# Kernel tuning notes

Hardware: AMD Instinct MI355X
Metric: run time of the kernel (lower is better)

## Reference

```python
import jax, jax.numpy as jnp
import numpy as np

N_NODES = 8_000_000
N_GRAPHS = 16384
OUT_DIM = 256
LABEL_MAX = 300  # some labels >= OUT_DIM to exercise the bounds check


def setup_inputs() -> dict:
    key = jax.random.key(0)
    k1, k2 = jax.random.split(key)
    x = jax.random.randint(k1, (N_NODES,), 0, LABEL_MAX, dtype=jnp.int32)
    # ptr: sorted segment boundaries with ptr[0]=0, ptr[-1]=N_NODES
    inner = jnp.sort(jax.random.randint(k2, (N_GRAPHS - 1,), 0, N_NODES, dtype=jnp.int32))
    ptr = jnp.concatenate([jnp.zeros((1,), jnp.int32), inner,
                           jnp.full((1,), N_NODES, jnp.int32)])
    node_weights = jnp.ones((N_NODES,), jnp.float32)  # all-ones -> plain counting
    return {"x": x, "ptr": ptr, "node_weights": node_weights,
            "num_graphs": N_GRAPHS, "out_dim": OUT_DIM}


def reference(x, ptr, node_weights, num_graphs, out_dim):
    # Segmented histogram: out[g, c] = # nodes in graph g with label c (c < out_dim).
    n = x.shape[0]
    # graph id of each node from CSR ptr boundaries
    seg = jnp.searchsorted(ptr, jnp.arange(n, dtype=ptr.dtype), side="right") - 1
    valid = x < out_dim
    xc = jnp.where(valid, x, 0)                 # clamp out-of-range labels
    w = jnp.where(valid, node_weights, 0.0)     # mask them out of the count
    out = jnp.zeros((num_graphs, out_dim), jnp.float32).at[seg, xc].add(w)
    return out
```

## Files before the change

### kernel.cpp

```cpp
#include <hip/hip_runtime.h>


extern "C" __global__ void seg_hist_kernel(const int* __restrict__ x,
                                           const int* __restrict__ ptr,
                                           const float* __restrict__ w,
                                           float* __restrict__ out,
                                           int out_dim) {
    extern __shared__ float hist[];

    const int g = blockIdx.x;
    const int start = ptr[g];
    const int end = ptr[g + 1];

    for (int c = threadIdx.x; c < out_dim; c += blockDim.x) hist[c] = 0.0f;
    __syncthreads();

    for (int i = start + (int)threadIdx.x; i < end; i += (int)blockDim.x) {
        const int lbl = x[i];
        if ((unsigned)lbl < (unsigned)out_dim) {
            atomicAdd(&hist[lbl], w[i]);
        }
    }
    __syncthreads();

    float* o = out + (size_t)g * (size_t)out_dim;
    for (int c = threadIdx.x; c < out_dim; c += blockDim.x) o[c] = hist[c];
}

extern "C" void kernel_launch(void* const* d_in, const int* in_sizes, int n_in,
                              void* d_out, int out_size, void* d_ws, size_t ws_size,
                              hipStream_t stream) {
    const int* x   = (const int*)d_in[0];
    const int* ptr = (const int*)d_in[1];
    const float* w = (const float*)d_in[2];
    float* out     = (float*)d_out;

    const int num_graphs = in_sizes[1] - 1;
    const int out_dim    = out_size / num_graphs;

    dim3 grid(num_graphs);
    dim3 block(256);
    size_t lds_bytes = (size_t)out_dim * sizeof(float);

    seg_hist_kernel<<<grid, block, lds_bytes, stream>>>(x, ptr, w, out, out_dim);
}
```

Baseline: 52.05 us.

## Partition histogram work by fixed node chunks with atomic merges at boundaries

Replaces the one-block-per-graph histogram with blocks that each own a fixed 2048-node chunk. A setup kernel binary-searches ptr for each chunk's starting graph and zeroes those rows. The main kernel stages x and w into LDS with vector loads, then walks the graphs overlapping its chunk. Graphs fully inside a chunk get their rows written directly; graphs cut by a chunk edge are merged with global atomics. This balances work regardless of segment sizes and widens loads, at the cost of an extra launch, per-graph barriers inside each chunk, and boundary atomics. A ws-size fallback keeps the old kernel.

```diff
diff --git a/kernel.cpp b/kernel.cpp
--- a/kernel.cpp
+++ b/kernel.cpp
@@ -1,30 +1,104 @@
 #include <hip/hip_runtime.h>
 
 
-extern "C" __global__ void seg_hist_kernel(const int* __restrict__ x,
-                                           const int* __restrict__ ptr,
-                                           const float* __restrict__ w,
-                                           float* __restrict__ out,
-                                           int out_dim) {
-    extern __shared__ float hist[];
+#define CHUNK   2048
+#define BLOCK_B 256
 
+extern "C" __global__ __launch_bounds__(64)
+void setup_kernel(const int* __restrict__ ptr, int* __restrict__ gstart,
+                  float* __restrict__ out, int n_nodes, int num_graphs,
+                  int out_dim) {
+    const int b = blockIdx.x;
+    long n0 = (long)b * CHUNK;
+    if (n0 > (long)n_nodes - 1) n0 = (long)n_nodes - 1;
+
+    int lo = 0, hi = num_graphs + 1;
+    while (lo < hi) {
+        const int mid = (lo + hi) >> 1;
+        if ((long)ptr[mid] <= n0) lo = mid + 1; else hi = mid;
+    }
+    const int g = lo - 1;
+
+    if (threadIdx.x == 0) gstart[b] = g;
+
+    float* row = out + (size_t)g * (size_t)out_dim;
+    for (int c = (int)threadIdx.x; c < out_dim; c += 64) row[c] = 0.0f;
+}
+
+extern "C" __global__ __launch_bounds__(BLOCK_B)
+void hist_kernel(const int* __restrict__ x, const int* __restrict__ ptr,
+                 const float* __restrict__ w, const int* __restrict__ gstart,
+                 float* __restrict__ out, int n_nodes, int out_dim) {
+    extern __shared__ char smem[];
+    int*   xbuf = (int*)smem;
+    float* wbuf = (float*)(smem + CHUNK * sizeof(int));
+    float* hist = (float*)(smem + CHUNK * sizeof(int) + CHUNK * sizeof(float));
+
+    const int b   = blockIdx.x;
+    const int t   = (int)threadIdx.x;
+    const int n0  = b * CHUNK;
+    const int n1  = min(n0 + CHUNK, n_nodes);
+    const int cnt = n1 - n0;
+
+    for (int base = 0; base < cnt; base += 4 * BLOCK_B) {
+        const int idx = base + t * 4;
+        if (idx + 4 <= cnt) {
+            *reinterpret_cast<int4*>(&xbuf[idx])   = *reinterpret_cast<const int4*>(&x[n0 + idx]);
+            *reinterpret_cast<float4*>(&wbuf[idx]) = *reinterpret_cast<const float4*>(&w[n0 + idx]);
+        } else if (idx < cnt) {
+            for (int k = idx; k < cnt; ++k) { xbuf[k] = x[n0 + k]; wbuf[k] = w[n0 + k]; }
+        }
+    }
+
+    const int g0 = gstart[b];
+    const int g1 = gstart[b + 1];
+    __syncthreads();
+
+    int pjs = ptr[g0];
+    for (int j = g0; j <= g1; ++j) {
+        const int pje = ptr[j + 1];
+        const int s = max(pjs, n0) - n0;
+        const int e = min(pje, n1) - n0;
+
+        for (int c = t; c < out_dim; c += BLOCK_B) hist[c] = 0.0f;
+        __syncthreads();
+
+        for (int i = s + t; i < e; i += BLOCK_B) {
+            const unsigned lbl = (unsigned)xbuf[i];
+            if (lbl < (unsigned)out_dim) atomicAdd(&hist[lbl], wbuf[i]);
+        }
+        __syncthreads();
+
+        float* row = out + (size_t)j * (size_t)out_dim;
+        if (j == g0 || j == g1) {
+            for (int c = t; c < out_dim; c += BLOCK_B) {
+                const float v = hist[c];
+                if (v != 0.0f) atomicAdd(&row[c], v);
+            }
+        } else {
+            for (int c = t; c < out_dim; c += BLOCK_B) row[c] = hist[c];
+        }
+        pjs = pje;
+    }
+}
+
+extern "C" __global__ __launch_bounds__(256)
+void seg_hist_fallback(const int* __restrict__ x, const int* __restrict__ ptr,
+                       const float* __restrict__ w, float* __restrict__ out,
+                       int out_dim) {
+    extern __shared__ float fhist[];
     const int g = blockIdx.x;
     const int start = ptr[g];
     const int end = ptr[g + 1];
-
-    for (int c = threadIdx.x; c < out_dim; c += blockDim.x) hist[c] = 0.0f;
+    for (int c = (int)threadIdx.x; c < out_dim; c += 256) fhist[c] = 0.0f;
     __syncthreads();
-
-    for (int i = start + (int)threadIdx.x; i < end; i += (int)blockDim.x) {
+    for (int i = start + (int)threadIdx.x; i < end; i += 256) {
         const int lbl = x[i];
-        if ((unsigned)lbl < (unsigned)out_dim) {
-            atomicAdd(&hist[lbl], w[i]);
-        }
+        if ((unsigned)lbl < (unsigned)out_dim) atomicAdd(&fhist[lbl], w[i]);
     }
     __syncthreads();
-
     float* o = out + (size_t)g * (size_t)out_dim;
-    for (int c = threadIdx.x; c < out_dim; c += blockDim.x) o[c] = hist[c];
+    for (int c = (int)threadIdx.x; c < out_dim; c += 256) o[c] = fhist[c];
 }
 
 extern "C" void kernel_launch(void* const* d_in, const int* in_sizes, int n_in,
@@ -35,12 +109,23 @@
     const float* w = (const float*)d_in[2];
     float* out     = (float*)d_out;
 
+    const int n_nodes    = in_sizes[0];
     const int num_graphs = in_sizes[1] - 1;
     const int out_dim    = out_size / num_graphs;
+    const int n_chunks   = (n_nodes + CHUNK - 1) / CHUNK;
 
-    dim3 grid(num_graphs);
-    dim3 block(256);
-    size_t lds_bytes = (size_t)out_dim * sizeof(float);
+    if (ws_size < (size_t)(n_chunks + 1) * sizeof(int)) {
+        seg_hist_fallback<<<num_graphs, 256, (size_t)out_dim * sizeof(float), stream>>>(
+            x, ptr, w, out, out_dim);
+        return;
+    }
 
-    seg_hist_kernel<<<grid, block, lds_bytes, stream>>>(x, ptr, w, out, out_dim);
+    int* gstart = (int*)d_ws;
+
+    setup_kernel<<<n_chunks + 1, 64, 0, stream>>>(ptr, gstart, out,
+                                                  n_nodes, num_graphs, out_dim);
+
+    const size_t lds = (size_t)CHUNK * 8 + (size_t)out_dim * sizeof(float);
+    hist_kernel<<<n_chunks, BLOCK_B, lds, stream>>>(x, ptr, w, gstart, out,
+                                                    n_nodes, out_dim);
 }
```

After: 57.45 us. +10.4%, slower.

## Partition nodes into fixed per-wave ranges with segment flush and double-buffered loads

Applied to the files above, without the earlier changes.

Replaces the one-block-per-graph kernel with a persistent grid where each wave takes a fixed 512-node range. The wave finds the owning graph by binary search over ptr using scalar loads, bins its nodes into a private LDS histogram, and writes each row directly when the graph lies wholly inside the range, otherwise merges it with global atomics. Vectorized int4/float4 loads are double-buffered across ranges, and the output is zeroed with a memset first. The aim is to remove the load imbalance from uneven segment sizes and to improve memory throughput, at the cost of an extra memset and boundary atomics.

```diff
diff --git a/kernel.cpp b/kernel.cpp
--- a/kernel.cpp
+++ b/kernel.cpp
@@ -1,30 +1,132 @@
 #include <hip/hip_runtime.h>
 
 
-extern "C" __global__ void seg_hist_kernel(const int* __restrict__ x,
-                                           const int* __restrict__ ptr,
-                                           const float* __restrict__ w,
-                                           float* __restrict__ out,
-                                           int out_dim) {
-    extern __shared__ float hist[];
+#define NPT   8
+#define WR    (64 * NPT)
+#define ODIM  256
+#define NBLK  1536
 
+__device__ __forceinline__ int sload_i32(const int* p, int idx) {
+    int v;
+    asm volatile("s_load_dword %0, %1, %2\n\ts_waitcnt lgkmcnt(0)"
+                 : "=&s"(v)
+                 : "s"(p), "s"(idx * 4));
+    return v;
+}
+
+#define LOADR(LA, LB, WA, WB, RR)                                              \
+    { const int _base = (RR) * WR + lane * NPT;                                \
+      if (_base + NPT <= n_nodes) {                                            \
+          LA = *reinterpret_cast<const int4*>(x + _base);                      \
+          LB = *reinterpret_cast<const int4*>(x + _base + 4);                  \
+          WA = *reinterpret_cast<const float4*>(w + _base);                    \
+          WB = *reinterpret_cast<const float4*>(w + _base + 4);                \
+      } else {                                                                 \
+          int _l[8]; float _w[8];                                              \
+          _Pragma("unroll")                                                    \
+          for (int _k = 0; _k < 8; ++_k) {                                     \
+              if (_base + _k < n_nodes) { _l[_k] = x[_base + _k];              \
+                                          _w[_k] = w[_base + _k]; }            \
+              else { _l[_k] = 0x7fffffff; _w[_k] = 0.0f; }                     \
+          }                                                                    \
+          LA = make_int4(_l[0], _l[1], _l[2], _l[3]);                          \
+          LB = make_int4(_l[4], _l[5], _l[6], _l[7]);                          \
+          WA = make_float4(_w[0], _w[1], _w[2], _w[3]);                        \
+          WB = make_float4(_w[4], _w[5], _w[6], _w[7]);                        \
+      } }
+
+#define ADDK(LBL, WV, K)                                                       \
+    { const int _n = nbase + (K);                                              \
+      if (_n >= s && _n < e && (unsigned)(LBL) < (unsigned)ODIM)               \
+          atomicAdd(&h[LBL], (WV)); }
+
+#define BINR(LA, LB, WA, WB, RR)                                               \
+    { const int r0 = __builtin_amdgcn_readfirstlane((RR) * WR);                \
+      const int r1 = min(r0 + WR, n_nodes);                                    \
+      const int nbase = r0 + lane * NPT;                                       \
+                  \
+      int lo = 0, hi = num_graphs - 1;                                         \
+      while (lo < hi) {                                                        \
+          const int mid = (lo + hi + 1) >> 1;                                  \
+          if (sload_i32(ptr, mid) <= r0) lo = mid; else hi = mid - 1;          \
+      }                                                                        \
+      int j = lo;                                                              \
+      int pstart = sload_i32(ptr, j);                                          \
+      for (;;) {                                                               \
+          const int pend = sload_i32(ptr, j + 1);                              \
+          const int s = max(pstart, r0);                                       \
+          const int e = min(pend, r1);                                         \
+          ADDK(LA.x, WA.x, 0) ADDK(LA.y, WA.y, 1)                              \
+          ADDK(LA.z, WA.z, 2) ADDK(LA.w, WA.w, 3)                              \
+          ADDK(LB.x, WB.x, 4) ADDK(LB.y, WB.y, 5)                              \
+          ADDK(LB.z, WB.z, 6) ADDK(LB.w, WB.w, 7)                              \
+          const bool whole = (pstart >= r0) && (pend <= r1);                   \
+          float* row = out + (size_t)j * ODIM;                                 \
+          _Pragma("unroll")                                                    \
+          for (int _k = 0; _k < 4; ++_k) {                                     \
+              const int bin = lane + 64 * _k;                                  \
+              const float v = h[bin];                                          \
+              if (whole)          row[bin] = v;                                \
+              else if (v != 0.0f) atomicAdd(&row[bin], v);                     \
+              h[bin] = 0.0f;                                                   \
+          }                                                                    \
+          if (pend >= r1) break;                                               \
+          ++j; pstart = pend;                                                  \
+      } }
+
+extern "C" __global__ __launch_bounds__(256, 6)
+void hist_kernel(const int* __restrict__ x, const int* __restrict__ ptr,
+                 const float* __restrict__ w, float* __restrict__ out,
+                 int n_nodes, int num_graphs) {
+    __shared__ float hist[4][ODIM];
+
+    const int wv   = (int)threadIdx.x >> 6;
+    const int lane = (int)threadIdx.x & 63;
+    float* h = hist[wv];
+
+#pragma unroll
+    for (int k = 0; k < 4; ++k) h[lane + 64 * k] = 0.0f;
+
+    const int n_ranges = (n_nodes + WR - 1) / WR;
+    const int stride   = NBLK * 4;
+    int r = (int)blockIdx.x * 4 + wv;
+
+    int4 la_a, lb_a, la_b, lb_b;
+    float4 wa_a, wb_a, wa_b, wb_b;
+
+    if (r < n_ranges) LOADR(la_a, lb_a, wa_a, wb_a, r);
+    bool useA = true;
+    while (r < n_ranges) {
+        const int rn = r + stride;
+        if (useA) {
+            if (rn < n_ranges) LOADR(la_b, lb_b, wa_b, wb_b, rn);
+            BINR(la_a, lb_a, wa_a, wb_a, r);
+        } else {
+            if (rn < n_ranges) LOADR(la_a, lb_a, wa_a, wb_a, rn);
+            BINR(la_b, lb_b, wa_b, wb_b, r);
+        }
+        useA = !useA;
+        r = rn;
+    }
+}
+
+extern "C" __global__ __launch_bounds__(256)
+void seg_hist_fallback(const int* __restrict__ x, const int* __restrict__ ptr,
+                       const float* __restrict__ w, float* __restrict__ out,
+                       int out_dim) {
+    extern __shared__ float fhist[];
     const int g = blockIdx.x;
     const int start = ptr[g];
     const int end = ptr[g + 1];
-
-    for (int c = threadIdx.x; c < out_dim; c += blockDim.x) hist[c] = 0.0f;
+    for (int c = (int)threadIdx.x; c < out_dim; c += 256) fhist[c] = 0.0f;
     __syncthreads();
-
-    for (int i = start + (int)threadIdx.x; i < end; i += (int)blockDim.x) {
+    for (int i = start + (int)threadIdx.x; i < end; i += 256) {
         const int lbl = x[i];
-        if ((unsigned)lbl < (unsigned)out_dim) {
-            atomicAdd(&hist[lbl], w[i]);
-        }
+        if ((unsigned)lbl < (unsigned)out_dim) atomicAdd(&fhist[lbl], w[i]);
     }
     __syncthreads();
-
     float* o = out + (size_t)g * (size_t)out_dim;
-    for (int c = threadIdx.x; c < out_dim; c += blockDim.x) o[c] = hist[c];
+    for (int c = (int)threadIdx.x; c < out_dim; c += 256) o[c] = fhist[c];
 }
 
 extern "C" void kernel_launch(void* const* d_in, const int* in_sizes, int n_in,
@@ -35,12 +137,17 @@
     const float* w = (const float*)d_in[2];
     float* out     = (float*)d_out;
 
+    const int n_nodes    = in_sizes[0];
     const int num_graphs = in_sizes[1] - 1;
     const int out_dim    = out_size / num_graphs;
 
-    dim3 grid(num_graphs);
-    dim3 block(256);
-    size_t lds_bytes = (size_t)out_dim * sizeof(float);
+    if (out_dim != ODIM) {
+        seg_hist_fallback<<<num_graphs, 256, (size_t)out_dim * sizeof(float), stream>>>(
+            x, ptr, w, out, out_dim);
+        return;
+    }
 
-    seg_hist_kernel<<<grid, block, lds_bytes, stream>>>(x, ptr, w, out, out_dim);
+    hipMemsetAsync(d_out, 0, (size_t)out_size * sizeof(float), stream);
+
+    hist_kernel<<<NBLK, 256, 0, stream>>>(x, ptr, w, out, n_nodes, num_graphs);
 }
```

Measured after the change: 59.60 us. +14.5%, slower.

## Split work into fixed node tiles per wavefront with per-wave LDS histograms

Applied to the files above, without the earlier changes.

Replaces one-block-per-graph scheduling with fixed 2048-node tiles, each handled by a single wavefront with its own LDS histogram. The wavefront finds the owning graph with a scalar binary search over ptr, then walks the segments inside its tile. A graph lying wholly inside a tile is written directly, while a boundary segment is merged into global memory with atomics after a memset of the output. The aim is to fix the load imbalance from uneven graph sizes and to use vectorized loads, at the cost of a memset launch, extra global atomics and per-segment flush overhead when tiles hold many small graphs.

```diff
diff --git a/kernel.cpp b/kernel.cpp
--- a/kernel.cpp
+++ b/kernel.cpp
@@ -1,30 +1,127 @@
 #include <hip/hip_runtime.h>
 
 
-extern "C" __global__ void seg_hist_kernel(const int* __restrict__ x,
-                                           const int* __restrict__ ptr,
-                                           const float* __restrict__ w,
-                                           float* __restrict__ out,
-                                           int out_dim) {
-    extern __shared__ float hist[];
+#define TILE  2048
+#define ODIM  256
 
+__device__ __forceinline__ int sload_i32(const int* p, int idx) {
+    const int off = __builtin_amdgcn_readfirstlane(idx * 4);
+    int v;
+    asm volatile("s_load_dword %0, %1, %2\n\ts_waitcnt lgkmcnt(0)"
+                 : "=&s"(v)
+                 : "s"(p), "s"(off));
+    return v;
+}
+
+extern "C" __global__ __launch_bounds__(256, 4)
+void hist_kernel(const int* __restrict__ x, const int* __restrict__ ptr,
+                 const float* __restrict__ w, float* __restrict__ out,
+                 int n_nodes, int num_graphs) {
+    __shared__ float hist[4][ODIM];
+
+    const int wv   = (int)threadIdx.x >> 6;
+    const int lane = (int)threadIdx.x & 63;
+    float* h = hist[wv];
+
+    const int n_tiles     = (n_nodes + TILE - 1) / TILE;
+    const int total_waves = (int)gridDim.x * 4;
+
+    for (int T = (int)blockIdx.x * 4 + wv; T < n_tiles; T += total_waves) {
+        const int A = __builtin_amdgcn_readfirstlane(T * TILE);
+        const int B = min(A + TILE, n_nodes);
+
+        int4   X[8];
+        float4 W[8];
+        const int labs = A + lane * 4;
+        if (B - A == TILE) {
+            #pragma unroll
+            for (int k = 0; k < 8; ++k) {
+                X[k] = *reinterpret_cast<const int4*>(x + labs + (k << 8));
+                W[k] = *reinterpret_cast<const float4*>(w + labs + (k << 8));
+            }
+        } else {
+            #pragma unroll
+            for (int k = 0; k < 8; ++k) {
+                int l[4]; float ww[4];
+                #pragma unroll
+                for (int m = 0; m < 4; ++m) {
+                    const int ii = labs + (k << 8) + m;
+                    if (ii < n_nodes) { l[m] = x[ii]; ww[m] = w[ii]; }
+                    else              { l[m] = 0x7fffffff; ww[m] = 0.0f; }
+                }
+                X[k] = make_int4(l[0], l[1], l[2], l[3]);
+                W[k] = make_float4(ww[0], ww[1], ww[2], ww[3]);
+            }
+        }
+        __builtin_amdgcn_sched_barrier(0);
+
+        #pragma unroll
+        for (int kk = 0; kk < 4; ++kk) h[lane + (kk << 6)] = 0.0f;
+
+        int lo = 0, hi = num_graphs - 1;
+        while (lo < hi) {
+            const int mid = (lo + hi + 1) >> 1;
+            if (sload_i32(ptr, mid) <= A) lo = mid; else hi = mid - 1;
+        }
+        int j = __builtin_amdgcn_readfirstlane(lo);
+        int pstart = sload_i32(ptr, j);
+
+        for (;;) {
+            const int pend = sload_i32(ptr, j + 1);
+            const int s = max(pstart, A);
+            const int e = min(pend, B);
+
+            if (s < e) {
+                #pragma unroll
+                for (int k = 0; k < 8; ++k) {
+                    const int i0 = labs + (k << 8);
+                    if (i0 < e && i0 + 4 > s) {
+#define ADDM(LBL, WV, M)                                                   \
+                        { const int ii = i0 + (M);                         \
+                          if (ii >= s && ii < e &&                         \
+                              (unsigned)(LBL) < (unsigned)ODIM)            \
+                              atomicAdd(&h[LBL], (WV)); }
+                        ADDM(X[k].x, W[k].x, 0) ADDM(X[k].y, W[k].y, 1)
+                        ADDM(X[k].z, W[k].z, 2) ADDM(X[k].w, W[k].w, 3)
+#undef ADDM
+                    }
+                }
+            }
+
+            const bool whole = (pstart >= A) && (pend <= B);
+            float* row = out + (size_t)j * ODIM;
+            #pragma unroll
+            for (int kk = 0; kk < 4; ++kk) {
+                const int bin = lane + (kk << 6);
+                const float v = h[bin];
+                if (whole)          row[bin] = v;
+                else if (v != 0.0f) atomicAdd(&row[bin], v);
+                h[bin] = 0.0f;
+            }
+
+            if (pend >= B) break;
+            ++j; pstart = pend;
+        }
+    }
+}
+
+extern "C" __global__ __launch_bounds__(256)
+void seg_hist_fallback(const int* __restrict__ x, const int* __restrict__ ptr,
+                       const float* __restrict__ w, float* __restrict__ out,
+                       int out_dim) {
+    extern __shared__ float fhist[];
     const int g = blockIdx.x;
     const int start = ptr[g];
     const int end = ptr[g + 1];
-
-    for (int c = threadIdx.x; c < out_dim; c += blockDim.x) hist[c] = 0.0f;
+    for (int c = (int)threadIdx.x; c < out_dim; c += 256) fhist[c] = 0.0f;
     __syncthreads();
-
-    for (int i = start + (int)threadIdx.x; i < end; i += (int)blockDim.x) {
+    for (int i = start + (int)threadIdx.x; i < end; i += 256) {
         const int lbl = x[i];
-        if ((unsigned)lbl < (unsigned)out_dim) {
-            atomicAdd(&hist[lbl], w[i]);
-        }
+        if ((unsigned)lbl < (unsigned)out_dim) atomicAdd(&fhist[lbl], w[i]);
     }
     __syncthreads();
-
     float* o = out + (size_t)g * (size_t)out_dim;
-    for (int c = threadIdx.x; c < out_dim; c += blockDim.x) o[c] = hist[c];
+    for (int c = (int)threadIdx.x; c < out_dim; c += 256) o[c] = fhist[c];
 }
 
 extern "C" void kernel_launch(void* const* d_in, const int* in_sizes, int n_in,
@@ -35,12 +132,19 @@
     const float* w = (const float*)d_in[2];
     float* out     = (float*)d_out;
 
+    const int n_nodes    = in_sizes[0];
     const int num_graphs = in_sizes[1] - 1;
     const int out_dim    = out_size / num_graphs;
 
-    dim3 grid(num_graphs);
-    dim3 block(256);
-    size_t lds_bytes = (size_t)out_dim * sizeof(float);
+    if (out_dim != ODIM) {
+        seg_hist_fallback<<<num_graphs, 256, (size_t)out_dim * sizeof(float), stream>>>(
+            x, ptr, w, out, out_dim);
+        return;
+    }
 
-    seg_hist_kernel<<<grid, block, lds_bytes, stream>>>(x, ptr, w, out, out_dim);
+    hipMemsetAsync(d_out, 0, (size_t)out_size * sizeof(float), stream);
+
+    const int n_tiles = (n_nodes + TILE - 1) / TILE;
+    const int n_blocks = (n_tiles + 3) / 4;
+    hist_kernel<<<n_blocks, 256, 0, stream>>>(x, ptr, w, out, n_nodes, num_graphs);
 }
```

After: 62.99 us. +21.0%, slower.
